# Kernel optimization log

Measured on AMD Instinct MI355X. Metric: run time of the kernel, lower is better.

## Reference

```python
import jax, jax.numpy as jnp
import numpy as np

FPN_SIZE = 512
TOTAL_SELECTS = 2048
NUM_JOINTS = TOTAL_SELECTS // 32  # 64
NUM_CLASSES = 200
BATCH = 128
BN_EPS = 1e-5


def setup_inputs() -> dict:
    key = jax.random.key(0)
    ks = jax.random.split(key, 12)
    C, N, J, K = FPN_SIZE, TOTAL_SELECTS, NUM_JOINTS, NUM_CLASSES
    Q = C // 4  # 128
    s = lambda *d: 1.0 / np.sqrt(d[-1])
    x = jax.random.normal(ks[0], (BATCH, N, C), dtype=jnp.float32)
    w_pool0 = jax.random.normal(ks[1], (J, N), dtype=jnp.float32) * s(N)
    b_pool0 = jnp.zeros((J,), dtype=jnp.float32)
    adj1 = jnp.eye(J, dtype=jnp.float32) / 100.0 + 1.0 / 100.0
    w_conv1 = jax.random.normal(ks[2], (C, C), dtype=jnp.float32) * s(C)
    b_conv1 = jnp.zeros((C,), dtype=jnp.float32)
    w_q = jax.random.normal(ks[3], (Q, C), dtype=jnp.float32) * s(C)
    b_q = jnp.zeros((Q,), dtype=jnp.float32)
    w_k = jax.random.normal(ks[4], (Q, C), dtype=jnp.float32) * s(C)
    b_k = jnp.zeros((Q,), dtype=jnp.float32)
    alpha1 = jnp.zeros((1,), dtype=jnp.float32) + 0.1  # small nonzero so attention path is exercised
    gamma = jnp.ones((C,), dtype=jnp.float32)
    beta = jnp.zeros((C,), dtype=jnp.float32)
    w_pool1 = jax.random.normal(ks[5], (1, J), dtype=jnp.float32) * s(J)
    b_pool1 = jnp.zeros((1,), dtype=jnp.float32)
    w_cls = jax.random.normal(ks[6], (K, C), dtype=jnp.float32) * s(C)
    b_cls = jnp.zeros((K,), dtype=jnp.float32)
    return dict(x=x, w_pool0=w_pool0, b_pool0=b_pool0, adj1=adj1,
                w_conv1=w_conv1, b_conv1=b_conv1, w_q=w_q, b_q=b_q,
                w_k=w_k, b_k=b_k, alpha1=alpha1, gamma=gamma, beta=beta,
                w_pool1=w_pool1, b_pool1=b_pool1, w_cls=w_cls, b_cls=b_cls)


def reference(x, w_pool0, b_pool0, adj1, w_conv1, b_conv1, w_q, b_q,
              w_k, b_k, alpha1, gamma, beta, w_pool1, b_pool1, w_cls, b_cls):
    # x: [B, N, C] -> transpose -> [B, C, N]
    hs = jnp.swapaxes(x, 1, 2)
    # param_pool0: Linear over last dim N -> J: [B, C, J]
    hs = jnp.einsum('bcn,jn->bcj', hs, w_pool0) + b_pool0
    # pointwise conv q/k projections then mean over channel dim -> [B, J]
    q1 = (jnp.einsum('bcj,qc->bqj', hs, w_q) + b_q[:, None]).mean(axis=1)
    k1 = (jnp.einsum('bcj,qc->bqj', hs, w_k) + b_k[:, None]).mean(axis=1)
    # outer-difference attention adjacency: [B, J, J]
    A1 = adj1 + jnp.tanh(q1[:, :, None] - k1[:, None, :]) * alpha1
    # conv1 (pointwise): [B, C, J]
    hs = jnp.einsum('bcj,oc->boj', hs, w_conv1) + b_conv1[:, None]
    # batched matmul with adjacency: [B, C, J]
    hs = jnp.einsum('bcj,bjk->bck', hs, A1)
    # BatchNorm1d over channels (batch statistics, biased var)
    mean = hs.mean(axis=(0, 2), keepdims=True)
    var = hs.var(axis=(0, 2), keepdims=True)
    hs = (hs - mean) * jax.lax.rsqrt(var + BN_EPS)
    hs = hs * gamma[None, :, None] + beta[None, :, None]
    # param_pool1: Linear J -> 1, flatten -> [B, C]
    hs = (jnp.einsum('bcj,oj->bco', hs, w_pool1) + b_pool1).reshape(hs.shape[0], -1)
    # classifier -> [B, num_classes]
    return hs @ w_cls.T + b_cls
```

## Files before the change

kernel.cpp:

```cpp
#include <hip/hip_runtime.h>

#define BB 128
#define NN 2048
#define CC 512
#define JJ 64
#define QQ 128
#define KK 200

using bf16x8  = __attribute__((ext_vector_type(8))) __bf16;
using floatx4 = __attribute__((ext_vector_type(4))) float;

__device__ __forceinline__ ushort f2bf(float f) {
    __bf16 h = (__bf16)f;
    return __builtin_bit_cast(ushort, h);
}

__device__ __forceinline__ bf16x8 ldg8(const ushort* p) {
    uint4 v = *(const uint4*)p;
    return __builtin_bit_cast(bf16x8, v);
}

__device__ __forceinline__ bf16x8 ldlds8(const ushort* p) {
    struct U4 { unsigned a, b, c, d; } v;
    v.a = *(const unsigned*)(p + 0);
    v.b = *(const unsigned*)(p + 2);
    v.c = *(const unsigned*)(p + 4);
    v.d = *(const unsigned*)(p + 6);
    return __builtin_bit_cast(bf16x8, v);
}

__global__ void k0_prep(const float* __restrict__ w_pool0, const float* __restrict__ w_conv1,
                        const float* __restrict__ w_cls, const float* __restrict__ w_q,
                        const float* __restrict__ b_q, const float* __restrict__ w_k,
                        const float* __restrict__ b_k,
                        ushort* __restrict__ w0b, ushort* __restrict__ wcb,
                        float* __restrict__ wclsT, float* __restrict__ wqm,
                        float* __restrict__ wkm, float* __restrict__ scal) {
    int gid = blockIdx.x * 256 + threadIdx.x;
    if (gid < JJ * NN) { w0b[gid] = f2bf(w_pool0[gid]); return; }
    gid -= JJ * NN;
    if (gid < CC * CC) { wcb[gid] = f2bf(w_conv1[gid]); return; }
    gid -= CC * CC;
    if (gid < CC * KK) {
        int c = gid / KK; int k = gid - c * KK;
        wclsT[gid] = w_cls[k * CC + c];
        return;
    }
    gid -= CC * KK;
    if (gid < 2 * CC) {
        int c = gid & (CC - 1);
        const float* src = (gid < CC) ? w_q : w_k;
        float s = 0.f;
        for (int q = 0; q < QQ; ++q) s += src[q * CC + c];
        ((gid < CC) ? wqm : wkm)[c] = s * (1.f / QQ);
        return;
    }
    gid -= 2 * CC;
    if (gid == 0) { float s = 0; for (int q = 0; q < QQ; ++q) s += b_q[q]; scal[0] = s * (1.f / QQ); }
    else if (gid == 1) { float s = 0; for (int q = 0; q < QQ; ++q) s += b_k[q]; scal[1] = s * (1.f / QQ); }
}

__global__ __launch_bounds__(256, 4) void k1_gemm(const float* __restrict__ x,
                                                  const float* __restrict__ b_pool0,
                                                  const ushort* __restrict__ w0b,
                                                  ushort* __restrict__ hsT) {
    __shared__ ushort xlds[64 * 34];
    __shared__ ushort outlds[64 * 66];

    const int blk = blockIdx.x;
    const int b = blk >> 3;
    const int c0 = (blk & 7) << 6;
    const int t = threadIdx.x;
    const int w = t >> 6, l = t & 63, lo = l & 15, quad = l >> 4;

    floatx4 acc[4];
#pragma unroll
    for (int m = 0; m < 4; ++m) acc[m] = (floatx4){0.f, 0.f, 0.f, 0.f};

    const int srow = t >> 5;
    const int scol = (t & 31) * 2;
    const float* xbase = x + (size_t)b * NN * CC + c0;

    for (int ks = 0; ks < NN / 32; ++ks) {
        const int k0 = ks * 32;
        __syncthreads();
#pragma unroll
        for (int r = 0; r < 4; ++r) {
            int n = srow + r * 8;
            const float2 v = *(const float2*)(xbase + (size_t)(k0 + n) * CC + scol);
            xlds[(scol + 0) * 34 + n] = f2bf(v.x);
            xlds[(scol + 1) * 34 + n] = f2bf(v.y);
        }
        __syncthreads();
        const int kk = k0 + quad * 8;
        bf16x8 afr[4];
#pragma unroll
        for (int m = 0; m < 4; ++m)
            afr[m] = ldg8(w0b + (size_t)(m * 16 + lo) * NN + kk);
        const bf16x8 bfr = ldlds8(xlds + (w * 16 + lo) * 34 + quad * 8);
#pragma unroll
        for (int m = 0; m < 4; ++m)
            acc[m] = __builtin_amdgcn_mfma_f32_16x16x32_bf16(afr[m], bfr, acc[m], 0, 0, 0);
    }

    __syncthreads();
#pragma unroll
    for (int m = 0; m < 4; ++m) {
#pragma unroll
        for (int r = 0; r < 4; ++r) {
            int j = m * 16 + quad * 4 + r;
            float v = acc[m][r] + b_pool0[j];
            outlds[j * 66 + w * 16 + lo] = f2bf(v);
        }
    }
    __syncthreads();
    const size_t obase = (size_t)b * JJ * CC + c0;
#pragma unroll
    for (int it = 0; it < 8; ++it) {
        int dwid = it * 256 + t;
        int j = dwid >> 5, cd = (dwid & 31) * 2;
        unsigned v = *(const unsigned*)(outlds + j * 66 + cd);
        *(unsigned*)(hsT + obase + (size_t)j * CC + cd) = v;
    }
}

__global__ __launch_bounds__(256) void k3_mid(const ushort* __restrict__ hsT,
                                              const ushort* __restrict__ wcb,
                                              const float* __restrict__ wqm,
                                              const float* __restrict__ wkm,
                                              const float* __restrict__ scal,
                                              const float* __restrict__ adj1,
                                              const float* __restrict__ alpha1,
                                              const float* __restrict__ b_conv1,
                                              const float* __restrict__ w_pool1,
                                              float* __restrict__ P,
                                              float* __restrict__ bn_sum,
                                              float* __restrict__ bn_sq) {
    __shared__ float q1s[64], k1s[64], w1s[64];
    __shared__ ushort a1t[64 * 66];
    __shared__ ushort lds2[128 * 66];

    const int blk = blockIdx.x;
    const int b = blk >> 2;
    const int o0 = (blk & 3) << 7;
    const int t = threadIdx.x;
    const int w = t >> 6, l = t & 63, lo = l & 15, quad = l >> 4;

    if (t < JJ) w1s[t] = w_pool1[t];

    floatx4 acc[4][2];
#pragma unroll
    for (int m = 0; m < 4; ++m)
#pragma unroll
        for (int u = 0; u < 2; ++u) acc[m][u] = (floatx4){0.f, 0.f, 0.f, 0.f};
    float qp[4] = {0.f, 0.f, 0.f, 0.f}, kp[4] = {0.f, 0.f, 0.f, 0.f};

    const ushort* hb = hsT + (size_t)b * JJ * CC;
    for (int ks = 0; ks < CC / 32; ++ks) {
        const int kk = ks * 32 + quad * 8;
        bf16x8 afr[4];
#pragma unroll
        for (int m = 0; m < 4; ++m)
            afr[m] = ldg8(hb + (size_t)(m * 16 + lo) * CC + kk);
        bf16x8 bfr[2];
#pragma unroll
        for (int u = 0; u < 2; ++u) {
            int o = o0 + w * 32 + u * 16 + lo;
            bfr[u] = ldg8(wcb + (size_t)o * CC + kk);
        }
        if (w == 0) {
            float wqv[8], wkv[8];
            *(float4*)&wqv[0] = *(const float4*)(wqm + kk);
            *(float4*)&wqv[4] = *(const float4*)(wqm + kk + 4);
            *(float4*)&wkv[0] = *(const float4*)(wkm + kk);
            *(float4*)&wkv[4] = *(const float4*)(wkm + kk + 4);
#pragma unroll
            for (int m = 0; m < 4; ++m)
#pragma unroll
                for (int i = 0; i < 8; ++i) {
                    float av = (float)afr[m][i];
                    qp[m] += av * wqv[i];
                    kp[m] += av * wkv[i];
                }
        }
#pragma unroll
        for (int m = 0; m < 4; ++m)
#pragma unroll
            for (int u = 0; u < 2; ++u)
                acc[m][u] = __builtin_amdgcn_mfma_f32_16x16x32_bf16(afr[m], bfr[u], acc[m][u], 0, 0, 0);
    }

    if (w == 0) {
#pragma unroll
        for (int m = 0; m < 4; ++m) {
            qp[m] += __shfl_xor(qp[m], 16); qp[m] += __shfl_xor(qp[m], 32);
            kp[m] += __shfl_xor(kp[m], 16); kp[m] += __shfl_xor(kp[m], 32);
        }
        if (t < 16) {
#pragma unroll
            for (int m = 0; m < 4; ++m) {
                q1s[m * 16 + lo] = qp[m] + scal[0];
                k1s[m * 16 + lo] = kp[m] + scal[1];
            }
        }
    }

    float bc[2];
#pragma unroll
    for (int u = 0; u < 2; ++u) bc[u] = b_conv1[o0 + w * 32 + u * 16 + lo];
#pragma unroll
    for (int m = 0; m < 4; ++m)
#pragma unroll
        for (int u = 0; u < 2; ++u)
#pragma unroll
            for (int r = 0; r < 4; ++r) {
                int jj = m * 16 + quad * 4 + r;
                int ol = w * 32 + u * 16 + lo;
                lds2[ol * 66 + jj] = f2bf(acc[m][u][r] + bc[u]);
            }
    __syncthreads();

    const float alpha = alpha1[0];
#pragma unroll
    for (int r = 0; r < 16; ++r) {
        int idx = r * 256 + t;
        int j = idx & 63, k = idx >> 6;
        float v = adj1[k * 64 + j] + tanhf(q1s[k] - k1s[j]) * alpha;
        a1t[j * 66 + k] = f2bf(v);
    }
    __syncthreads();

    floatx4 acc2[4][2];
#pragma unroll
    for (int m = 0; m < 4; ++m)
#pragma unroll
        for (int u = 0; u < 2; ++u) acc2[m][u] = (floatx4){0.f, 0.f, 0.f, 0.f};
#pragma unroll
    for (int ks = 0; ks < 2; ++ks) {
        const int kb = ks * 32 + quad * 8;
        bf16x8 a2[4];
#pragma unroll
        for (int m = 0; m < 4; ++m)
            a2[m] = ldlds8(a1t + (m * 16 + lo) * 66 + kb);
        bf16x8 b2[2];
#pragma unroll
        for (int u = 0; u < 2; ++u)
            b2[u] = ldlds8(lds2 + (w * 32 + u * 16 + lo) * 66 + kb);
#pragma unroll
        for (int m = 0; m < 4; ++m)
#pragma unroll
            for (int u = 0; u < 2; ++u)
                acc2[m][u] = __builtin_amdgcn_mfma_f32_16x16x32_bf16(a2[m], b2[u], acc2[m][u], 0, 0, 0);
    }

#pragma unroll
    for (int u = 0; u < 2; ++u) {
        int o = o0 + w * 32 + u * 16 + lo;
        float s1 = 0.f, s2 = 0.f, pv = 0.f;
#pragma unroll
        for (int m = 0; m < 4; ++m)
#pragma unroll
            for (int r = 0; r < 4; ++r) {
                float v = acc2[m][u][r];
                s1 += v; s2 += v * v;
                pv += v * w1s[m * 16 + quad * 4 + r];
            }
        s1 += __shfl_xor(s1, 16); s1 += __shfl_xor(s1, 32);
        s2 += __shfl_xor(s2, 16); s2 += __shfl_xor(s2, 32);
        pv += __shfl_xor(pv, 16); pv += __shfl_xor(pv, 32);
        if (quad == 0) {
            atomicAdd(&bn_sum[o], s1);
            atomicAdd(&bn_sq[o], s2);
            P[b * CC + o] = pv;
        }
    }
}

__global__ __launch_bounds__(256) void k4_cls(const float* __restrict__ P,
                                              const float* __restrict__ bn_sum,
                                              const float* __restrict__ bn_sq,
                                              const float* __restrict__ gamma,
                                              const float* __restrict__ beta,
                                              const float* __restrict__ w_pool1,
                                              const float* __restrict__ b_pool1,
                                              const float* __restrict__ wclsT,
                                              const float* __restrict__ b_cls,
                                              float* __restrict__ out) {
    __shared__ float pooled[CC];
    __shared__ float w1s[JJ];
    const int b = blockIdx.x;
    const int t = threadIdx.x;
    if (t < JJ) w1s[t] = w_pool1[t];
    __syncthreads();
    float S1 = 0.f;
#pragma unroll
    for (int j = 0; j < JJ; ++j) S1 += w1s[j];
    const float inv = 1.f / (BB * JJ);
    for (int c = t; c < CC; c += 256) {
        float mean = bn_sum[c] * inv;
        float var = bn_sq[c] * inv - mean * mean;
        float g = gamma[c] * rsqrtf(var + 1e-5f);
        float h = (beta[c] - g * mean) * S1 + b_pool1[0];
        pooled[c] = g * P[b * CC + c] + h;
    }
    __syncthreads();
    if (t < KK) {
        float acc = b_cls[t];
        for (int c = 0; c < CC; ++c) acc += pooled[c] * wclsT[c * KK + t];
        out[b * KK + t] = acc;
    }
}

static constexpr size_t OFF_BNSUM = 0;
static constexpr size_t OFF_BNSQ  = 2048;
static constexpr size_t OFF_SCAL  = 4096;
static constexpr size_t OFF_WQM   = 4352;
static constexpr size_t OFF_WKM   = 6400;
static constexpr size_t OFF_W0B   = 8448;
static constexpr size_t OFF_WCB   = 270592;
static constexpr size_t OFF_WCLST = 794880;
static constexpr size_t OFF_HST   = 1204480;
static constexpr size_t OFF_P     = 9593088;

extern "C" void kernel_launch(void* const* d_in, const int* in_sizes, int n_in,
                              void* d_out, int out_size, void* d_ws, size_t ws_size,
                              hipStream_t stream) {
    const float* x       = (const float*)d_in[0];
    const float* w_pool0 = (const float*)d_in[1];
    const float* b_pool0 = (const float*)d_in[2];
    const float* adj1    = (const float*)d_in[3];
    const float* w_conv1 = (const float*)d_in[4];
    const float* b_conv1 = (const float*)d_in[5];
    const float* w_q     = (const float*)d_in[6];
    const float* b_q     = (const float*)d_in[7];
    const float* w_k     = (const float*)d_in[8];
    const float* b_k     = (const float*)d_in[9];
    const float* alpha1  = (const float*)d_in[10];
    const float* gamma   = (const float*)d_in[11];
    const float* beta    = (const float*)d_in[12];
    const float* w_pool1 = (const float*)d_in[13];
    const float* b_pool1 = (const float*)d_in[14];
    const float* w_cls   = (const float*)d_in[15];
    const float* b_cls   = (const float*)d_in[16];

    char* ws = (char*)d_ws;
    float*  bn_sum = (float*)(ws + OFF_BNSUM);
    float*  bn_sq  = (float*)(ws + OFF_BNSQ);
    float*  scal   = (float*)(ws + OFF_SCAL);
    float*  wqm    = (float*)(ws + OFF_WQM);
    float*  wkm    = (float*)(ws + OFF_WKM);
    ushort* w0b    = (ushort*)(ws + OFF_W0B);
    ushort* wcb    = (ushort*)(ws + OFF_WCB);
    float*  wclsT  = (float*)(ws + OFF_WCLST);
    ushort* hsT    = (ushort*)(ws + OFF_HST);
    float*  P      = (float*)(ws + OFF_P);
    float*  out    = (float*)d_out;

    hipMemsetAsync(ws, 0, 4096, stream);
    k0_prep<<<1941, 256, 0, stream>>>(w_pool0, w_conv1, w_cls, w_q, b_q, w_k, b_k,
                                      w0b, wcb, wclsT, wqm, wkm, scal);
    k1_gemm<<<BB * 8, 256, 0, stream>>>(x, b_pool0, w0b, hsT);
    k3_mid<<<BB * 4, 256, 0, stream>>>(hsT, wcb, wqm, wkm, scal, adj1, alpha1,
                                       b_conv1, w_pool1, P, bn_sum, bn_sq);
    k4_cls<<<BB, 256, 0, stream>>>(P, bn_sum, bn_sq, gamma, beta, w_pool1, b_pool1,
                                   wclsT, b_cls, out);
}
```

Before: 823.0 us.

## Double-buffer x tiles and widen k1 GEMM block to 128 channels

Rewrites the pool0 GEMM kernel so each block covers 128 channels instead of 64, halving the number of blocks and reusing each A fragment from w0b across two MFMA B tiles. The x tile is now loaded with float4 reads into registers for the next step while the current step computes, then packed as bf16 pairs into a double-buffered LDS array, leaving one barrier per iteration. This aims to hide global load latency for x, the main memory stream, and to cut redundant w0b loads. In exchange it uses more registers and fewer blocks (512), which may reduce occupancy and latency hiding.

```diff
diff --git a/kernel.cpp b/kernel.cpp
--- a/kernel.cpp
+++ b/kernel.cpp
@@ -60,67 +60,99 @@
     else if (gid == 1) { float s = 0; for (int q = 0; q < QQ; ++q) s += b_k[q]; scal[1] = s * (1.f / QQ); }
 }
 
-__global__ __launch_bounds__(256, 4) void k1_gemm(const float* __restrict__ x,
-                                                  const float* __restrict__ b_pool0,
-                                                  const ushort* __restrict__ w0b,
-                                                  ushort* __restrict__ hsT) {
-    __shared__ ushort xlds[64 * 34];
-    __shared__ ushort outlds[64 * 66];
+__global__ __launch_bounds__(256) void k1_gemm(const float* __restrict__ x,
+                                               const float* __restrict__ b_pool0,
+                                               const ushort* __restrict__ w0b,
+                                               ushort* __restrict__ hsT) {
+    __shared__ unsigned xs[2][128 * 17];
 
     const int blk = blockIdx.x;
-    const int b = blk >> 3;
-    const int c0 = (blk & 7) << 6;
+    const int b = blk >> 2;
+    const int c0 = (blk & 3) << 7;
     const int t = threadIdx.x;
     const int w = t >> 6, l = t & 63, lo = l & 15, quad = l >> 4;
 
-    floatx4 acc[4];
-#pragma unroll
-    for (int m = 0; m < 4; ++m) acc[m] = (floatx4){0.f, 0.f, 0.f, 0.f};
-
-    const int srow = t >> 5;
-    const int scol = (t & 31) * 2;
-    const float* xbase = x + (size_t)b * NN * CC + c0;
+    const int cq = t & 31;
+    const int nb = t >> 5;
+
+    floatx4 acc[4][2];
+#pragma unroll
+    for (int m = 0; m < 4; ++m)
+#pragma unroll
+        for (int u = 0; u < 2; ++u) acc[m][u] = (floatx4){0.f, 0.f, 0.f, 0.f};
+
+    const float* xb = x + (size_t)b * NN * CC + c0 + 4 * cq;
+
+    float4 ra[2], rb[2];
+    auto issue = [&](int n0) {
+#pragma unroll
+        for (int p = 0; p < 2; ++p) {
+            const int pi = nb + p * 8;
+            ra[p] = *(const float4*)(xb + (size_t)(n0 + 2 * pi) * CC);
+            rb[p] = *(const float4*)(xb + (size_t)(n0 + 2 * pi + 1) * CC);
+        }
+    };
+    auto commit = [&](int buf) {
+#pragma unroll
+        for (int p = 0; p < 2; ++p) {
+            const int pi = nb + p * 8;
+#pragma unroll
+            for (int j = 0; j < 4; ++j) {
+                unsigned lo16 = f2bf(((const float*)&ra[p])[j]);
+                unsigned hi16 = f2bf(((const float*)&rb[p])[j]);
+                xs[buf][(4 * cq + j) * 17 + pi] = lo16 | (hi16 << 16);
+            }
+        }
+    };
+
+    issue(0);
+    commit(0);
+    __syncthreads();
 
     for (int ks = 0; ks < NN / 32; ++ks) {
-        const int k0 = ks * 32;
+        const int cur = ks & 1;
+        if (ks < NN / 32 - 1) issue((ks + 1) * 32);
+
+        const int kk = ks * 32 + quad * 8;
+        bf16x8 afr[4];
+#pragma unroll
+        for (int m = 0; m < 4; ++m)
+            afr[m] = ldg8(w0b + (size_t)(m * 16 + lo) * NN + kk);
+        bf16x8 bfr[2];
+#pragma unroll
+        for (int u = 0; u < 2; ++u)
+            bfr[u] = ldlds8((const ushort*)&xs[cur][(w * 32 + u * 16 + lo) * 17] + quad * 8);
+#pragma unroll
+        for (int m = 0; m < 4; ++m)
+#pragma unroll
+            for (int u = 0; u < 2; ++u)
+                acc[m][u] = __builtin_amdgcn_mfma_f32_16x16x32_bf16(afr[m], bfr[u], acc[m][u], 0, 0, 0);
+
+        if (ks < NN / 32 - 1) commit(cur ^ 1);
         __syncthreads();
-#pragma unroll
-        for (int r = 0; r < 4; ++r) {
-            int n = srow + r * 8;
-            const float2 v = *(const float2*)(xbase + (size_t)(k0 + n) * CC + scol);
-            xlds[(scol + 0) * 34 + n] = f2bf(v.x);
-            xlds[(scol + 1) * 34 + n] = f2bf(v.y);
-        }
-        __syncthreads();
-        const int kk = k0 + quad * 8;
-        bf16x8 afr[4];
-#pragma unroll
-        for (int m = 0; m < 4; ++m)
-            afr[m] = ldg8(w0b + (size_t)(m * 16 + lo) * NN + kk);
-        const bf16x8 bfr = ldlds8(xlds + (w * 16 + lo) * 34 + quad * 8);
-#pragma unroll
-        for (int m = 0; m < 4; ++m)
-            acc[m] = __builtin_amdgcn_mfma_f32_16x16x32_bf16(afr[m], bfr, acc[m], 0, 0, 0);
-    }
-
-    __syncthreads();
+    }
+
+    ushort* outl = (ushort*)&xs[0][0];
 #pragma unroll
     for (int m = 0; m < 4; ++m) {
-#pragma unroll
-        for (int r = 0; r < 4; ++r) {
-            int j = m * 16 + quad * 4 + r;
-            float v = acc[m][r] + b_pool0[j];
-            outlds[j * 66 + w * 16 + lo] = f2bf(v);
-        }
+        const float4 bias = *(const float4*)(b_pool0 + m * 16 + quad * 4);
+#pragma unroll
+        for (int u = 0; u < 2; ++u)
+#pragma unroll
+            for (int r = 0; r < 4; ++r) {
+                int j = m * 16 + quad * 4 + r;
+                int cl = w * 32 + u * 16 + lo;
+                outl[j * 130 + cl] = f2bf(acc[m][u][r] + ((const float*)&bias)[r]);
+            }
     }
     __syncthreads();
     const size_t obase = (size_t)b * JJ * CC + c0;
 #pragma unroll
-    for (int it = 0; it < 8; ++it) {
+    for (int it = 0; it < 16; ++it) {
         int dwid = it * 256 + t;
-        int j = dwid >> 5, cd = (dwid & 31) * 2;
-        unsigned v = *(const unsigned*)(outlds + j * 66 + cd);
-        *(unsigned*)(hsT + obase + (size_t)j * CC + cd) = v;
+        int j = dwid >> 6, cd = dwid & 63;
+        unsigned v = ((const unsigned*)outl)[j * 65 + cd];
+        *(unsigned*)(hsT + obase + (size_t)j * CC + 2 * cd) = v;
     }
 }
 
@@ -359,7 +391,7 @@
     hipMemsetAsync(ws, 0, 4096, stream);
     k0_prep<<<1941, 256, 0, stream>>>(w_pool0, w_conv1, w_cls, w_q, b_q, w_k, b_k,
                                       w0b, wcb, wclsT, wqm, wkm, scal);
-    k1_gemm<<<BB * 8, 256, 0, stream>>>(x, b_pool0, w0b, hsT);
+    k1_gemm<<<BB * 4, 256, 0, stream>>>(x, b_pool0, w0b, hsT);
     k3_mid<<<BB * 4, 256, 0, stream>>>(hsT, wcb, wqm, wkm, scal, adj1, alpha1,
                                        b_conv1, w_pool1, P, bn_sum, bn_sq);
     k4_cls<<<BB, 256, 0, stream>>>(P, bn_sum, bn_sq, gamma, beta, w_pool1, b_pool1,
```

After: 770.0 us. 1.07x faster.
